# Kernel optimization log

Measured on AMD Instinct MI355X. Metric: run time of the kernel, lower is better.

## Reference

```python
import jax, jax.numpy as jnp
import numpy as np

B, HIMG, WIMG = 8, 24, 24
WIDTH, NCH, CW = 1024, 8, 128
NHEADS, HD = 8, 16
HALF = HD // 2
NFREQ, VOCAB, NCLS = 32, 256, 10
HIDDEN = 4096
EPS = 1e-6
LAMBDA_INIT = 0.8 - 0.6 * float(np.exp(-0.3 * 0.0))  # layer_idx = 0


def rmsnorm(x, w, eps=EPS):
    return x * jax.lax.rsqrt(jnp.mean(x * x, axis=-1, keepdims=True) + eps) * w


def causal_attn(q, k, v, scale):
    # q,k: [B,H,L,d2], v: [B,H,L,D]
    L = q.shape[2]
    scores = jnp.einsum('bhqd,bhkd->bhqk', q, k) * scale
    mask = jnp.tril(jnp.ones((L, L), dtype=bool))
    scores = jnp.where(mask, scores, -jnp.inf)
    return jnp.einsum('bhqk,bhkd->bhqd', jax.nn.softmax(scores, axis=-1), v)


def diff_attn(h, qkv_w, qkv_b, qn_w, kn_w, hn_w, lq1, lk1, lq2, lk2, ow, ob):
    Bb, L, C = h.shape
    qkv = jax.nn.silu(h @ qkv_w + qkv_b).reshape(Bb, L, 3, NHEADS, HD)
    q, k, v = qkv[:, :, 0], qkv[:, :, 1], qkv[:, :, 2]
    t = lambda a: a.transpose(0, 2, 1, 3)  # [B,L,H,d] -> [B,H,L,d]
    q1 = t(rmsnorm(q[..., :HALF], qn_w)); q2 = t(rmsnorm(q[..., HALF:], qn_w))
    k1 = t(rmsnorm(k[..., :HALF], kn_w)); k2 = t(rmsnorm(k[..., HALF:], kn_w))
    v = t(v)
    lam = jnp.exp(jnp.dot(lq1, lk1)) - jnp.exp(jnp.dot(lq2, lk2)) + LAMBDA_INIT
    scale = 1.0 / np.sqrt(HALF)
    out1 = causal_attn(q1, k1, v, scale)
    out2 = causal_attn(q2, k2, v, scale)
    diff = rmsnorm(out1 - lam * out2, hn_w) * (1.0 - LAMBDA_INIT)
    out = diff.transpose(0, 2, 1, 3).reshape(Bb, L, C)
    return jax.nn.silu(out @ ow + ob)


def setup_inputs() -> dict:
    key = jax.random.key(0)
    ks = iter(jax.random.split(key, 64))
    n = lambda shape, s=0.02: jax.random.normal(next(ks), shape, jnp.float32) * s
    return dict(
        x=jax.random.uniform(next(ks), (B, HIMG, WIMG), jnp.float32),
        top_k=4,
        pixel_embed=n((VOCAB, WIDTH)),
        freq_h=n((NFREQ,), 0.1), freq_w=n((NFREQ,), 0.1),
        phase_h=jnp.zeros((NFREQ,), jnp.float32), phase_w=jnp.zeros((NFREQ,), jnp.float32),
        pos_proj_w=n((4 * NFREQ, WIDTH)), pos_proj_b=jnp.zeros((WIDTH,), jnp.float32),
        embed_norm_w=jnp.ones((WIDTH,), jnp.float32),
        se_w1=n((WIDTH, WIDTH // 4)), se_b1=jnp.zeros((WIDTH // 4,), jnp.float32),
        se_w2=n((WIDTH // 4, WIDTH)), se_b2=jnp.zeros((WIDTH,), jnp.float32),
        mix_norm_w=jnp.ones((WIDTH,), jnp.float32),
        mlp_w1=n((WIDTH, HIDDEN)), mlp_b1=jnp.zeros((HIDDEN,), jnp.float32),
        mlp_w2=n((HIDDEN, WIDTH)), mlp_b2=jnp.zeros((WIDTH,), jnp.float32),
        mlp_norm_w=jnp.ones((WIDTH,), jnp.float32),
        router_w=n((WIDTH, NCH)), router_b=jnp.zeros((NCH,), jnp.float32),
        qkv_w=n((NCH, CW, 3 * CW)), qkv_b=jnp.zeros((NCH, 3 * CW), jnp.float32),
        q_norm_w=jnp.ones((NCH, HALF), jnp.float32), k_norm_w=jnp.ones((NCH, HALF), jnp.float32),
        head_norm_w=jnp.ones((NCH, HD), jnp.float32),
        lam_q1=n((NCH, HALF), 0.1), lam_k1=n((NCH, HALF), 0.1),
        lam_q2=n((NCH, HALF), 0.1), lam_k2=n((NCH, HALF), 0.1),
        out_w=n((NCH, CW, CW)), out_b=jnp.zeros((NCH, CW), jnp.float32),
        seg_norm_w=jnp.ones((NCH, CW), jnp.float32),
        head_w=n((WIDTH, NCLS)), head_b=jnp.zeros((NCLS,), jnp.float32),
    )


def reference(x, top_k, pixel_embed, freq_h, freq_w, phase_h, phase_w, pos_proj_w,
              pos_proj_b, embed_norm_w, se_w1, se_b1, se_w2, se_b2, mix_norm_w,
              mlp_w1, mlp_b1, mlp_w2, mlp_b2, mlp_norm_w, router_w, router_b,
              qkv_w, qkv_b, q_norm_w, k_norm_w, head_norm_w, lam_q1, lam_k1,
              lam_q2, lam_k2, out_w, out_b, seg_norm_w, head_w, head_b):
    Bb, H, W = x.shape
    L = H * W
    # LearnedSinusoidal2DEmbed
    hp = jnp.arange(H, dtype=jnp.float32) / H
    wp = jnp.arange(W, dtype=jnp.float32) / W
    fh = jax.nn.softplus(freq_h) * 10.0
    fw = jax.nn.softplus(freq_w) * 10.0
    ha = hp[:, None] * fh + phase_h          # [H, NFREQ]
    wa = wp[:, None] * fw + phase_w
    h_enc = jnp.concatenate([jnp.sin(ha), jnp.cos(ha)], -1)
    w_enc = jnp.concatenate([jnp.sin(wa), jnp.cos(wa)], -1)
    pos = jnp.concatenate([jnp.broadcast_to(h_enc[:, None], (H, W, 2 * NFREQ)),
                           jnp.broadcast_to(w_enc[None, :], (H, W, 2 * NFREQ))], -1)
    pos = pos @ pos_proj_w + pos_proj_b      # [H, W, WIDTH]
    xi = jnp.clip((x * 255.0).astype(jnp.int32), 0, 255).reshape(Bb, L)
    h = pixel_embed[xi] + pos.reshape(1, L, WIDTH)
    h = rmsnorm(h, embed_norm_w)
    # ChannelMixer: SE + RMSNorm residual, MLP residual, top-k router
    s = jnp.mean(h, axis=1)
    s = jax.nn.sigmoid(jax.nn.silu(s @ se_w1 + se_b1) @ se_w2 + se_b2)
    h = h + rmsnorm(h * s[:, None, :] - h, mix_norm_w)
    h = h + rmsnorm(jax.nn.silu(h @ mlp_w1 + mlp_b1) @ mlp_w2 + mlp_b2, mlp_norm_w)
    logits_r = jnp.mean(h, axis=1) @ router_w + router_b   # [B, NCH]
    tv, ti = jax.lax.top_k(logits_r, top_k)
    rw = jnp.zeros_like(logits_r).at[jnp.arange(Bb)[:, None], ti].set(jax.nn.softmax(tv, axis=-1))
    # ChannelSegment: per-channel differential attention expert, routed
    outs = []
    for i in range(NCH):
        hi = h[..., i * CW:(i + 1) * CW]
        o = diff_attn(hi, qkv_w[i], qkv_b[i], q_norm_w[i], k_norm_w[i], head_norm_w[i],
                      lam_q1[i], lam_k1[i], lam_q2[i], lam_k2[i], out_w[i], out_b[i])
        hi = hi + rmsnorm(o, seg_norm_w[i])
        outs.append(hi * rw[:, i][:, None, None])
    h = jnp.concatenate(outs, axis=-1)
    # classifier head
    return jnp.mean(h, axis=1) @ head_w + head_b
```

## Files before the change

kernel.cpp:

```cpp
#include <hip/hip_runtime.h>
#include <math.h>

typedef __bf16 bf16;
typedef __bf16 bf16x8 __attribute__((ext_vector_type(8)));
typedef __bf16 bf16x4 __attribute__((ext_vector_type(4)));
typedef __bf16 bf16x2 __attribute__((ext_vector_type(2)));
typedef float f32x4 __attribute__((ext_vector_type(4)));
typedef short s16x4 __attribute__((ext_vector_type(4)));

constexpr int Bsz = 8, HIMG = 24, WIMG = 24;
constexpr int Lq = 576;
constexpr int WIDTH = 1024, NCH = 8, CW = 128;
constexpr int NHEADS = 8, HD = 16, HALF = 8;
constexpr float EPS = 1e-6f;
constexpr float LAMINIT = 0.2f;
constexpr float QSCALE_E = 0.35355339059327373f * 1.4426950408889634f;
constexpr int ROWS = Bsz * Lq;
constexpr long PSTRIDE = 4718592;

__device__ __forceinline__ float fexp2(float x) {
#if __has_builtin(__builtin_amdgcn_exp2f)
  return __builtin_amdgcn_exp2f(x);
#else
  return exp2f(x);
#endif
}

constexpr size_t B_HB    = 0;
constexpr size_t B_G2B   = B_HB    + 9437184;
constexpr size_t B_ENCB  = B_G2B   + 9437184;
constexpr size_t B_POSWT = B_ENCB  + 163840;
constexpr size_t B_QKVWT = B_POSWT + 262144;
constexpr size_t B_OWT   = B_QKVWT + 786432;
constexpr size_t B_SE    = B_OWT   + 262144;
constexpr size_t B_T1    = B_SE    + 32768;
constexpr size_t B_MP    = B_T1    + 8192;
constexpr size_t B_RW    = B_MP    + 524288;
constexpr size_t B_LAM   = B_RW    + 256;
constexpr size_t B_POOL  = B_LAM   + 256;
constexpr size_t WS_BIG  = B_POOL + 8388608 + 8388608 + 37748736;
constexpr size_t WS_BIG2 = WS_BIG + 9437184;
constexpr size_t WS_BIG3 = WS_BIG + 4 * 9437184;

__device__ __forceinline__ float blockReduceSum256(float v, float* red) {
  #pragma unroll
  for (int off = 32; off; off >>= 1) v += __shfl_down(v, off, 64);
  int lane = threadIdx.x & 63, wid = threadIdx.x >> 6;
  if (lane == 0) red[wid] = v;
  __syncthreads();
  float total = 0.f;
  #pragma unroll
  for (int i = 0; i < 4; i++) total += red[i];
  return total;
}
__device__ __forceinline__ float silu(float x) { return x / (1.f + __expf(-x)); }

__device__ __forceinline__ void gl16(const bf16* g, bf16* l) {
  __builtin_amdgcn_global_load_lds(
      (const __attribute__((address_space(1))) void*)g,
      (__attribute__((address_space(3))) void*)l, 16, 0, 0);
}

__device__ __forceinline__ f32x4 mfma16(bf16x4 a, bf16x4 b, f32x4 c) {
#if __has_builtin(__builtin_amdgcn_mfma_f32_16x16x16bf16_1k)
  union { bf16x4 h; s16x4 s; } ua, ub;
  ua.h = a; ub.h = b;
  return __builtin_amdgcn_mfma_f32_16x16x16bf16_1k(ua.s, ub.s, c, 0, 0, 0);
#else
  f32x4 d = c;
  asm volatile("v_mfma_f32_16x16x16_bf16 %0, %1, %2, %0"
               : "+v"(d) : "v"(a), "v"(b));
  return d;
#endif
}

__device__ __forceinline__ void tcast_tile(const float* __restrict__ W,
    bf16* __restrict__ Wt, int K, int N, long zo, int bx, int by) {
  __shared__ float t[32][33];
  int n0 = bx * 32, k0 = by * 32;
  int tid = threadIdx.x;
  int r = tid >> 3, c4 = (tid & 7) * 4;
  const float4 v = *(const float4*)(W + zo + (long)(k0 + r) * N + n0 + c4);
  t[c4 + 0][r] = v.x; t[c4 + 1][r] = v.y; t[c4 + 2][r] = v.z; t[c4 + 3][r] = v.w;
  __syncthreads();
  bf16* dst = Wt + zo + (long)(n0 + r) * K + k0 + c4;
  dst[0] = (bf16)t[r][c4 + 0]; dst[1] = (bf16)t[r][c4 + 1];
  dst[2] = (bf16)t[r][c4 + 2]; dst[3] = (bf16)t[r][c4 + 3];
}

__global__ __launch_bounds__(256) void k_tcast_all(
    const float* __restrict__ w1, const float* __restrict__ w2,
    const float* __restrict__ posw, const float* __restrict__ qkvw,
    const float* __restrict__ outw,
    bf16* __restrict__ W1T, bf16* __restrict__ W2T, bf16* __restrict__ POSWT,
    bf16* __restrict__ QKVWT, bf16* __restrict__ OWT) {
  int bid = blockIdx.x;
  if (bid < 4096) {
    tcast_tile(w1, W1T, 1024, 4096, 0, bid % 128, bid / 128);
  } else if (bid < 8192) {
    int t = bid - 4096;
    tcast_tile(w2, W2T, 4096, 1024, 0, t % 32, t / 32);
  } else if (bid < 8320) {
    int t = bid - 8192;
    tcast_tile(posw, POSWT, 128, 1024, 0, t % 32, t / 32);
  } else if (bid < 8704) {
    int t = bid - 8320;
    int z = t / 48; t -= z * 48;
    tcast_tile(qkvw, QKVWT, 128, 384, (long)z * 49152, t % 12, t / 12);
  } else {
    int t = bid - 8704;
    int z = t / 16; t -= z * 16;
    tcast_tile(outw, OWT, 128, 128, (long)z * 16384, t % 4, t / 4);
  }
}

__global__ void k_enc_b(const float* __restrict__ fh, const float* __restrict__ fw,
                        const float* __restrict__ ph, const float* __restrict__ pw,
                        bf16* __restrict__ enc) {
  int idx = blockIdx.x * blockDim.x + threadIdx.x;
  if (idx >= Lq * 128) return;
  int l = idx >> 7, c = idx & 127;
  int hh = l / WIMG, ww = l % WIMG;
  float v;
  if (c < 64) {
    int f = c & 31;
    float fr = log1pf(__expf(fh[f])) * 10.f;
    float a = (hh / (float)HIMG) * fr + ph[f];
    v = (c < 32) ? sinf(a) : cosf(a);
  } else {
    int f = c & 31;
    float fr = log1pf(__expf(fw[f])) * 10.f;
    float a = (ww / (float)WIMG) * fr + pw[f];
    v = (c < 96) ? sinf(a) : cosf(a);
  }
  enc[idx] = (bf16)v;
}

template <int ACT, int OUTBF, int SWZ>
__global__ __launch_bounds__(256) void gemm_bt(
    const bf16* __restrict__ A, int lda, long aZs,
    const bf16* __restrict__ Bt, int ldb, long bZs,
    const float* __restrict__ bias, int biasZs,
    void* __restrict__ Cv, int ldc, long cZs,
    int M, int N, int K) {
  __shared__ bf16 As[128 * 32];
  __shared__ bf16 Bs[128 * 32];
  int tid = threadIdx.x;
  int m0, n0, z;
  if constexpr (SWZ == 0) {
    m0 = blockIdx.y * 128; n0 = blockIdx.x * 128; z = blockIdx.z;
  } else if constexpr (SWZ == 1) {
    int lid = blockIdx.x;
    int xcd = lid & 7, idx = lid >> 3;
    int j = idx & 15, G = xcd + 8 * (idx >> 4);
    m0 = (G % 36) * 128; n0 = ((G / 36) * 16 + j) * 128; z = 0;
  } else {
    int lid = blockIdx.x;
    int xcd = lid & 7, idx = lid >> 3;
    int n = idx & 7, G = xcd + 8 * (idx >> 3);
    m0 = (G % 36) * 128; n0 = n * 128; z = G / 36;
  }
  const bf16* Ab = A + (long)z * aZs;
  const bf16* Bb = Bt + (long)z * bZs;
  f32x4 acc[4][4] = {};
  int wv = tid >> 6, lane = tid & 63;
  int wrow = (wv >> 1) * 64, wcol = (wv & 1) * 64;
  int lm = lane & 15, lq = lane >> 4;
  const bf16* ag = Ab + (long)(m0 + (tid >> 2)) * lda + (tid & 3) * 8;
  const bf16* bg = Bb + (long)(n0 + (tid >> 2)) * ldb + (tid & 3) * 8;
  bf16* asd = As + tid * 8;
  bf16* bsd = Bs + tid * 8;
  for (int k0 = 0; k0 < K; k0 += 32) {
    gl16(ag + k0, asd);
    gl16(ag + k0 + 64L * lda, asd + 2048);
    gl16(bg + k0, bsd);
    gl16(bg + k0 + 64L * ldb, bsd + 2048);
    __syncthreads();
    bf16x8 af[4], bfr[4];
    #pragma unroll
    for (int i = 0; i < 4; i++) {
      af[i]  = *(const bf16x8*)(As + (wrow + i * 16 + lm) * 32 + lq * 8);
      bfr[i] = *(const bf16x8*)(Bs + (wcol + i * 16 + lm) * 32 + lq * 8);
    }
    #pragma unroll
    for (int i = 0; i < 4; i++)
      #pragma unroll
      for (int j = 0; j < 4; j++)
        acc[i][j] = __builtin_amdgcn_mfma_f32_16x16x32_bf16(af[i], bfr[j], acc[i][j], 0, 0, 0);
    __syncthreads();
  }
  long cz = (long)z * cZs;
  const float* bz = bias ? bias + (long)z * biasZs : nullptr;
  #pragma unroll
  for (int i = 0; i < 4; i++) {
    int row = m0 + wrow + i * 16 + lq * 4;
    #pragma unroll
    for (int j = 0; j < 4; j++) {
      int col = n0 + wcol + j * 16 + lm;
      float bv = bz ? bz[col] : 0.f;
      #pragma unroll
      for (int r = 0; r < 4; r++) {
        float v = acc[i][j][r] + bv;
        if (ACT == 1) v = silu(v);
        long off = cz + (long)(row + r) * ldc + col;
        if (OUTBF) ((bf16*)Cv)[off] = (bf16)v;
        else       ((float*)Cv)[off] = v;
      }
    }
  }
}

template <int ACT, int OUTBF, int ACC, int NORM>
__global__ __launch_bounds__(256) void gemm64(
    const bf16* __restrict__ A, int lda, long aZs,
    const bf16* __restrict__ Bt, int ldb, long bZs,
    const float* __restrict__ bias, int biasZs,
    void* __restrict__ Cv, int ldc, long cZs,
    int M, int N, int K,
    const float* __restrict__ qn, const float* __restrict__ kn) {
  __shared__ bf16 As[64 * 32];
  __shared__ bf16 Bs[128 * 32];
  int tid = threadIdx.x;
  int m0 = blockIdx.y * 64, n0 = blockIdx.x * 128;
  int z = blockIdx.z;
  const bf16* Ab = A + (long)z * aZs;
  const bf16* Bb = Bt + (long)z * bZs;
  f32x4 acc[4][2] = {};
  int wv = tid >> 6, lane = tid & 63;
  int lm = lane & 15, lq = lane >> 4;
  int wcol = wv * 32;
  const bf16* ag = Ab + (long)(m0 + (tid >> 2)) * lda + (tid & 3) * 8;
  const bf16* bg = Bb + (long)(n0 + (tid >> 2)) * ldb + (tid & 3) * 8;
  bf16* asd = As + tid * 8;
  bf16* bsd = Bs + tid * 8;
  for (int k0 = 0; k0 < K; k0 += 32) {
    gl16(ag + k0, asd);
    gl16(bg + k0, bsd);
    gl16(bg + k0 + 64L * ldb, bsd + 2048);
    __syncthreads();
    bf16x8 af[4], bfr[2];
    #pragma unroll
    for (int i = 0; i < 4; i++)
      af[i] = *(const bf16x8*)(As + (i * 16 + lm) * 32 + lq * 8);
    #pragma unroll
    for (int j = 0; j < 2; j++)
      bfr[j] = *(const bf16x8*)(Bs + (wcol + j * 16 + lm) * 32 + lq * 8);
    #pragma unroll
    for (int i = 0; i < 4; i++)
      #pragma unroll
      for (int j = 0; j < 2; j++)
        acc[i][j] = __builtin_amdgcn_mfma_f32_16x16x32_bf16(af[i], bfr[j], acc[i][j], 0, 0, 0);
    __syncthreads();
  }
  long cz = (long)z * cZs;
  const float* bz = bias ? bias + (long)z * biasZs : nullptr;
  if constexpr (NORM == 0) {
    #pragma unroll
    for (int i = 0; i < 4; i++) {
      int row = m0 + i * 16 + lq * 4;
      #pragma unroll
      for (int j = 0; j < 2; j++) {
        int col = n0 + wcol + j * 16 + lm;
        float bv = bz ? bz[col] : 0.f;
        #pragma unroll
        for (int r = 0; r < 4; r++) {
          float v = acc[i][j][r] + bv;
          long off = cz + (long)(row + r) * ldc + col;
          if (ACC) v += (float)((bf16*)Cv)[off];
          if (ACT == 1) v = silu(v);
          if (OUTBF) ((bf16*)Cv)[off] = (bf16)v;
          else       ((float*)Cv)[off] = v;
        }
      }
    }
  } else {
    int nsec = blockIdx.x;
    bool don = nsec < 2;
    float wnv = 1.f;
    if (nsec == 0) wnv = qn[z * 8 + (lm & 7)] * QSCALE_E;
    else if (nsec == 1) wnv = kn[z * 8 + (lm & 7)];
    #pragma unroll
    for (int i = 0; i < 4; i++) {
      int row = m0 + i * 16 + lq * 4;
      #pragma unroll
      for (int j = 0; j < 2; j++) {
        int col = n0 + wcol + j * 16 + lm;
        float bv = bz ? bz[col] : 0.f;
        #pragma unroll
        for (int r = 0; r < 4; r++) {
          float v = acc[i][j][r] + bv;
          if (ACT == 1) v = silu(v);
          float s = v * v;
          s += __shfl_xor(s, 1);
          s += __shfl_xor(s, 2);
          s += __shfl_xor(s, 4);
          if (don) v = v * rsqrtf(s * 0.125f + EPS) * wnv;
          ((bf16*)Cv)[cz + (long)(row + r) * ldc + col] = (bf16)v;
        }
      }
    }
  }
}

__global__ __launch_bounds__(256) void k_embed(const float* __restrict__ x,
    const float* __restrict__ emb, const float* __restrict__ pos,
    const float* __restrict__ nw, bf16* __restrict__ h) {
  __shared__ float red[4];
  int row = blockIdx.x;
  int l = row % Lq;
  int xi = (int)(x[row] * 255.f);
  xi = min(max(xi, 0), 255);
  const float* er = emb + (long)xi * WIDTH;
  const float* pr = pos + (long)l * WIDTH;
  int c0 = threadIdx.x * 4;
  float v[4]; float ss = 0.f;
  #pragma unroll
  for (int i = 0; i < 4; i++) { v[i] = er[c0 + i] + pr[c0 + i]; ss += v[i] * v[i]; }
  ss = blockReduceSum256(ss, red);
  float r = rsqrtf(ss / WIDTH + EPS);
  bf16* hr = h + (long)row * WIDTH;
  #pragma unroll
  for (int i = 0; i < 4; i++) hr[c0 + i] = (bf16)(v[i] * r * nw[c0 + i]);
}

__global__ void k_meanl_p(const bf16* __restrict__ h, float* __restrict__ part) {
  int lp = blockIdx.x, b = blockIdx.y, t = threadIdx.x;
  const bf16* p = h + ((long)b * Lq + (long)lp * 36) * WIDTH + t * 4;
  float a0 = 0, a1 = 0, a2 = 0, a3 = 0;
  for (int l = 0; l < 36; l++) {
    bf16x4 v = *(const bf16x4*)(p + (long)l * WIDTH);
    a0 += (float)v[0]; a1 += (float)v[1]; a2 += (float)v[2]; a3 += (float)v[3];
  }
  float* dst = part + ((long)b * 16 + lp) * WIDTH + t * 4;
  dst[0] = a0; dst[1] = a1; dst[2] = a2; dst[3] = a3;
}

__global__ __launch_bounds__(256) void k_se1(const float* __restrict__ part,
    const float* __restrict__ w1, const float* __restrict__ b1,
    float* __restrict__ t1) {
  __shared__ float sv[1024];
  __shared__ float red[256];
  int jb = blockIdx.x, b = blockIdx.y, t = threadIdx.x;
  for (int c = t; c < 1024; c += 256) {
    float a = 0.f;
    #pragma unroll
    for (int lp = 0; lp < 16; lp++) a += part[((long)b * 16 + lp) * 1024 + c];
    sv[c] = a * (1.f / 576.f);
  }
  __syncthreads();
  int j = t & 7, pt = t >> 3;
  int j0 = jb * 8;
  float acc = 0.f;
  int c0 = pt * 32;
  #pragma unroll 8
  for (int c = c0; c < c0 + 32; c++) acc += sv[c] * w1[c * 256 + j0 + j];
  red[t] = acc;
  __syncthreads();
  if (t < 8) {
    float a = b1[j0 + t];
    #pragma unroll
    for (int p = 0; p < 32; p++) a += red[p * 8 + t];
    t1[b * 256 + j0 + t] = silu(a);
  }
}

__global__ __launch_bounds__(256) void k_se2(const float* __restrict__ t1,
    const float* __restrict__ w2, const float* __restrict__ b2,
    float* __restrict__ s) {
  __shared__ float red[256];
  int jb = blockIdx.x, b = blockIdx.y, t = threadIdx.x;
  int j = t & 31, pt = t >> 5;
  int j0 = jb * 32;
  const float* tb = t1 + b * 256;
  float acc = 0.f;
  int c0 = pt * 32;
  #pragma unroll 8
  for (int c = c0; c < c0 + 32; c++) acc += tb[c] * w2[c * 1024 + j0 + j];
  red[t] = acc;
  __syncthreads();
  if (t < 32) {
    float a = b2[j0 + t];
    #pragma unroll
    for (int p = 0; p < 8; p++) a += red[p * 32 + t];
    s[b * 1024 + j0 + t] = 1.f / (1.f + __expf(-a));
  }
}

__global__ __launch_bounds__(256) void k_mix_b(bf16* __restrict__ h,
    const float* __restrict__ s, const float* __restrict__ mw) {
  __shared__ float red[4];
  int row = blockIdx.x;
  int b = row / Lq;
  bf16* hr = h + (long)row * WIDTH;
  const float* sb = s + b * WIDTH;
  int c0 = threadIdx.x * 4;
  float hv[4], y[4]; float ss = 0.f;
  #pragma unroll
  for (int i = 0; i < 4; i++) {
    hv[i] = (float)hr[c0 + i];
    y[i] = hv[i] * (sb[c0 + i] - 1.f); ss += y[i] * y[i];
  }
  ss = blockReduceSum256(ss, red);
  float r = rsqrtf(ss / WIDTH + EPS);
  #pragma unroll
  for (int i = 0; i < 4; i++) hr[c0 + i] = (bf16)(hv[i] + y[i] * r * mw[c0 + i]);
}

__global__ __launch_bounds__(256) void k_addnorm_b(bf16* __restrict__ h,
    const bf16* __restrict__ g, const float* __restrict__ mw) {
  __shared__ float red[4];
  int row = blockIdx.x;
  bf16* hr = h + (long)row * WIDTH;
  const bf16* gr = g + (long)row * WIDTH;
  int c0 = threadIdx.x * 4;
  float y[4]; float ss = 0.f;
  #pragma unroll
  for (int i = 0; i < 4; i++) { y[i] = (float)gr[c0 + i]; ss += y[i] * y[i]; }
  ss = blockReduceSum256(ss, red);
  float r = rsqrtf(ss / WIDTH + EPS);
  #pragma unroll
  for (int i = 0; i < 4; i++)
    hr[c0 + i] = (bf16)((float)hr[c0 + i] + y[i] * r * mw[c0 + i]);
}

__global__ __launch_bounds__(256) void k_addnorm2(bf16* __restrict__ h,
    const bf16* __restrict__ p0, const bf16* __restrict__ p1,
    const float* __restrict__ b2, const float* __restrict__ mw) {
  __shared__ float red[4];
  int row = blockIdx.x;
  bf16* hr = h + (long)row * WIDTH;
  const bf16* g0 = p0 + (long)row * WIDTH;
  const bf16* g1 = p1 + (long)row * WIDTH;
  int c0 = threadIdx.x * 4;
  float y[4]; float ss = 0.f;
  #pragma unroll
  for (int i = 0; i < 4; i++) {
    y[i] = (float)g0[c0 + i] + (float)g1[c0 + i] + b2[c0 + i];
    ss += y[i] * y[i];
  }
  ss = blockReduceSum256(ss, red);
  float r = rsqrtf(ss / WIDTH + EPS);
  #pragma unroll
  for (int i = 0; i < 4; i++)
    hr[c0 + i] = (bf16)((float)hr[c0 + i] + y[i] * r * mw[c0 + i]);
}

__global__ __launch_bounds__(256) void k_addnorm4(bf16* __restrict__ h,
    const bf16* __restrict__ parts, const float* __restrict__ b2,
    const float* __restrict__ mw) {
  __shared__ float red[4];
  int row = blockIdx.x;
  bf16* hr = h + (long)row * WIDTH;
  const bf16* g0 = parts + (long)row * WIDTH;
  int c0 = threadIdx.x * 4;
  float y[4]; float ss = 0.f;
  #pragma unroll
  for (int i = 0; i < 4; i++) {
    float a = b2[c0 + i];
    #pragma unroll
    for (int p = 0; p < 4; p++) a += (float)g0[(long)p * PSTRIDE + c0 + i];
    y[i] = a; ss += a * a;
  }
  ss = blockReduceSum256(ss, red);
  float r = rsqrtf(ss / WIDTH + EPS);
  #pragma unroll
  for (int i = 0; i < 4; i++)
    hr[c0 + i] = (bf16)((float)hr[c0 + i] + y[i] * r * mw[c0 + i]);
}

__global__ __launch_bounds__(256) void k_router(const float* __restrict__ part,
    const float* __restrict__ rwgt, const float* __restrict__ rb,
    const float* __restrict__ lq1, const float* __restrict__ lk1,
    const float* __restrict__ lq2, const float* __restrict__ lk2,
    float* __restrict__ rw, float* __restrict__ lam) {
  __shared__ float sv[1024];
  __shared__ float red[256];
  __shared__ float lg[8];
  int b = blockIdx.x, t = threadIdx.x;
  for (int c = t; c < 1024; c += 256) {
    float a = 0.f;
    #pragma unroll
    for (int lp = 0; lp < 16; lp++) a += part[((long)b * 16 + lp) * 1024 + c];
    sv[c] = a * (1.f / 576.f);
  }
  __syncthreads();
  int j = t & 7, pt = t >> 3;
  float acc = 0.f;
  int c0 = pt * 32;
  #pragma unroll 8
  for (int c = c0; c < c0 + 32; c++) acc += sv[c] * rwgt[c * 8 + j];
  red[t] = acc;
  __syncthreads();
  if (t < 8) {
    float a = rb[t];
    for (int p = 0; p < 32; p++) a += red[p * 8 + t];
    lg[t] = a;
  }
  __syncthreads();
  if (t == 0) {
    float v[8]; bool sel[8];
    #pragma unroll
    for (int i = 0; i < 8; i++) { v[i] = lg[i]; sel[i] = false; }
    int idxs[4]; float vals[4];
    for (int s = 0; s < 4; s++) {
      int bi = -1; float bv = -1e30f;
      for (int i = 0; i < 8; i++) if (!sel[i] && v[i] > bv) { bv = v[i]; bi = i; }
      sel[bi] = true; idxs[s] = bi; vals[s] = bv;
    }
    float m = vals[0], den = 0.f, e[4];
    for (int s = 0; s < 4; s++) { e[s] = __expf(vals[s] - m); den += e[s]; }
    for (int i = 0; i < 8; i++) rw[b * 8 + i] = 0.f;
    for (int s = 0; s < 4; s++) rw[b * 8 + idxs[s]] = e[s] / den;
  }
  if (b == 0 && t >= 8 && t < 16) {
    int c = t - 8;
    float d1 = 0.f, d2 = 0.f;
    for (int i = 0; i < 8; i++) {
      d1 += lq1[c * 8 + i] * lk1[c * 8 + i];
      d2 += lq2[c * 8 + i] * lk2[c * 8 + i];
    }
    lam[c] = __expf(d1) - __expf(d2) + LAMINIT;
  }
}

__global__ __launch_bounds__(256) void k_attn_mfma(
    const bf16* __restrict__ qkv, const float* __restrict__ lam,
    const float* __restrict__ hnw, bf16* __restrict__ dc) {
  __shared__ bf16 Ks[576 * 16];
  __shared__ bf16 Vt[16 * 584];
  int tid = threadIdx.x;
  int slice = blockIdx.x; int zc = slice >> 3, b = slice & 7;
  int head = blockIdx.z;
  const bf16* qkvb = qkv + ((long)zc * ROWS + (long)b * Lq) * 384;
  for (int i = tid; i < 1152; i += 256) {
    int row = i >> 1, hf = i & 1;
    gl16(qkvb + (long)row * 384 + 128 + head * 16 + hf * 8, Ks + i * 8);
  }
  for (int i = tid; i < 1152; i += 256) {
    int row = i >> 1, dh = i & 1;
    bf16x8 v = *(const bf16x8*)(qkvb + (long)row * 384 + 256 + head * 16 + dh * 8);
    #pragma unroll
    for (int j = 0; j < 8; j++) Vt[(dh * 8 + j) * 584 + row] = v[j];
  }
  __syncthreads();
  int wv = tid >> 6, lane = tid & 63;
  int lm = lane & 15, lq = lane >> 4;
  float lamv = lam[zc];
  float hwv[4];
  #pragma unroll
  for (int r = 0; r < 4; r++) hwv[r] = hnw[zc * 16 + lq * 4 + r] * (1.f - LAMINIT);
  int u = blockIdx.y * 4 + wv;
  int prA, prB, prC;
  if (u < 6) { prA = u + 2; prB = 17 - u; prC = -1; }
  else       { int v2 = u - 6; prA = v2; prB = 8 + v2; prC = 11 - v2; }
  for (int pi = 0; pi < 3; pi++) {
    int pr = (pi == 0) ? prA : (pi == 1) ? prB : prC;
    if (pr < 0) continue;
    bf16x8 bq0[2] = {{}, {}}, bq1[2] = {{}, {}};
    if (lq < 2) {
      #pragma unroll
      for (int tile = 0; tile < 2; tile++) {
        bf16x8 t8 = *(const bf16x8*)(
            qkvb + (long)(pr * 32 + tile * 16 + lm) * 384 + head * 16 + lq * 8);
        if (lq == 0) bq0[tile] = t8; else bq1[tile] = t8;
      }
    }
    f32x4 o[2][2] = {};
    float den[2][2] = {};
    for (int kc = 0; kc <= pr; kc++) {
      f32x4 sT[2][2][2] = {};
      #pragma unroll
      for (int t = 0; t < 2; t++) {
        bf16x8 aK = {};
        if (lq < 2) aK = *(const bf16x8*)(Ks + (kc * 32 + t * 16 + lm) * 16 + lq * 8);
        #pragma unroll
        for (int tile = 0; tile < 2; tile++) {
          sT[t][tile][0] = __builtin_amdgcn_mfma_f32_16x16x32_bf16(aK, bq0[tile], sT[t][tile][0], 0, 0, 0);
          sT[t][tile][1] = __builtin_amdgcn_mfma_f32_16x16x32_bf16(aK, bq1[tile], sT[t][tile][1], 0, 0, 0);
        }
      }
      bool diag = (kc == pr);
      #pragma unroll
      for (int t = 0; t < 2; t++) {
        bf16x4 aV = *(const bf16x4*)(Vt + lm * 584 + kc * 32 + t * 16 + lq * 4);
        #pragma unroll
        for (int tile = 0; tile < 2; tile++) {
          if (diag && tile == 0 && t == 1) continue;
          bool masked = diag && (tile == t);
          #pragma unroll
          for (int h2 = 0; h2 < 2; h2++) {
            bf16x4 pb;
            float dsum = 0.f;
            #pragma unroll
            for (int r = 0; r < 4; r++) {
              float ev = fexp2(sT[t][tile][h2][r]);
              if (masked && (lq * 4 + r > lm)) ev = 0.f;
              dsum += ev;
              pb[r] = (bf16)ev;
            }
            den[tile][h2] += dsum;
            o[tile][h2] = mfma16(aV, pb, o[tile][h2]);
          }
        }
      }
    }
    #pragma unroll
    for (int tile = 0; tile < 2; tile++)
      #pragma unroll
      for (int h2 = 0; h2 < 2; h2++) {
        den[tile][h2] += __shfl_xor(den[tile][h2], 16);
        den[tile][h2] += __shfl_xor(den[tile][h2], 32);
      }
    #pragma unroll
    for (int tile = 0; tile < 2; tile++) {
      float inv1 = 1.f / den[tile][0];
      float inv2 = lamv / den[tile][1];
      float dff[4]; float ss = 0.f;
      #pragma unroll
      for (int r = 0; r < 4; r++) {
        dff[r] = o[tile][0][r] * inv1 - o[tile][1][r] * inv2;
        ss += dff[r] * dff[r];
      }
      ss += __shfl_xor(ss, 16);
      ss += __shfl_xor(ss, 32);
      float rr = rsqrtf(ss * 0.0625f + EPS);
      bf16x4 outp;
      #pragma unroll
      for (int r = 0; r < 4; r++) outp[r] = (bf16)(dff[r] * rr * hwv[r]);
      long rowg = (long)zc * ROWS + (long)b * Lq + pr * 32 + tile * 16 + lm;
      *(bf16x4*)(dc + rowg * 128 + head * 16 + lq * 4) = outp;
    }
  }
}

__global__ __launch_bounds__(64) void k_segpool(const bf16* __restrict__ h,
    const bf16* __restrict__ op, const float* __restrict__ segw,
    const float* __restrict__ rw, float* __restrict__ part) {
  int lp = blockIdx.x, b = blockIdx.y, ch = blockIdx.z;
  int t = threadIdx.x;
  int c0 = t * 2;
  float w0 = segw[ch * 128 + c0], w1 = segw[ch * 128 + c0 + 1];
  float rwv = rw[b * 8 + ch];
  float a0 = 0.f, a1 = 0.f;
  for (int l = 0; l < 36; l++) {
    int row = b * Lq + lp * 36 + l;
    const bf16* oprow = op + (long)ch * ROWS * CW + (long)row * CW;
    bf16x2 yv = *(const bf16x2*)(oprow + c0);
    float y0 = (float)yv[0], y1 = (float)yv[1];
    float ss = y0 * y0 + y1 * y1;
    #pragma unroll
    for (int m = 1; m < 64; m <<= 1) ss += __shfl_xor(ss, m);
    float r = rsqrtf(ss * (1.f / 128.f) + EPS);
    bf16x2 hv = *(const bf16x2*)(h + (long)row * WIDTH + ch * 128 + c0);
    a0 += ((float)hv[0] + y0 * r * w0) * rwv;
    a1 += ((float)hv[1] + y1 * r * w1) * rwv;
  }
  float* dst = part + ((long)b * 16 + lp) * 1024 + ch * 128 + c0;
  dst[0] = a0; dst[1] = a1;
}

__global__ __launch_bounds__(256) void k_head(const float* __restrict__ part,
    const float* __restrict__ hw, const float* __restrict__ hb, float* __restrict__ out) {
  __shared__ float pool[1024];
  __shared__ float red[256];
  int b = blockIdx.x, t = threadIdx.x;
  for (int c = t; c < 1024; c += 256) {
    float a = 0.f;
    #pragma unroll
    for (int lp = 0; lp < 16; lp++) a += part[((long)b * 16 + lp) * 1024 + c];
    pool[c] = a * (1.f / 576.f);
  }
  __syncthreads();
  int j = t & 15, pt = t >> 4;
  float acc = 0.f;
  if (j < 10)
    for (int c = pt * 64; c < pt * 64 + 64; c++)
      acc += pool[c] * hw[c * 10 + j];
  red[t] = acc;
  __syncthreads();
  if (t < 10) {
    float a = hb[t];
    for (int p = 0; p < 16; p++) a += red[p * 16 + t];
    out[b * 10 + t] = a;
  }
}

extern "C" void kernel_launch(void* const* d_in, const int* in_sizes, int n_in,
                              void* d_out, int out_size, void* d_ws, size_t ws_size,
                              hipStream_t stream) {
  const float* x          = (const float*)d_in[0];
  const float* pixel_embed= (const float*)d_in[2];
  const float* freq_h     = (const float*)d_in[3];
  const float* freq_w     = (const float*)d_in[4];
  const float* phase_h    = (const float*)d_in[5];
  const float* phase_w    = (const float*)d_in[6];
  const float* pos_proj_w = (const float*)d_in[7];
  const float* pos_proj_b = (const float*)d_in[8];
  const float* embed_norm = (const float*)d_in[9];
  const float* se_w1      = (const float*)d_in[10];
  const float* se_b1      = (const float*)d_in[11];
  const float* se_w2      = (const float*)d_in[12];
  const float* se_b2      = (const float*)d_in[13];
  const float* mix_norm   = (const float*)d_in[14];
  const float* mlp_w1     = (const float*)d_in[15];
  const float* mlp_b1     = (const float*)d_in[16];
  const float* mlp_w2     = (const float*)d_in[17];
  const float* mlp_b2     = (const float*)d_in[18];
  const float* mlp_norm   = (const float*)d_in[19];
  const float* router_w   = (const float*)d_in[20];
  const float* router_b   = (const float*)d_in[21];
  const float* qkv_w      = (const float*)d_in[22];
  const float* qkv_b      = (const float*)d_in[23];
  const float* q_norm_w   = (const float*)d_in[24];
  const float* k_norm_w   = (const float*)d_in[25];
  const float* head_norm_w= (const float*)d_in[26];
  const float* lam_q1     = (const float*)d_in[27];
  const float* lam_k1     = (const float*)d_in[28];
  const float* lam_q2     = (const float*)d_in[29];
  const float* lam_k2     = (const float*)d_in[30];
  const float* out_w      = (const float*)d_in[31];
  const float* out_b      = (const float*)d_in[32];
  const float* seg_norm_w = (const float*)d_in[33];
  const float* head_w     = (const float*)d_in[34];
  const float* head_b     = (const float*)d_in[35];

  char* W = (char*)d_ws;
  bf16*  HB    = (bf16*)(W + B_HB);
  bf16*  G2B   = (bf16*)(W + B_G2B);
  float* POS   = (float*)(W + B_G2B);
  bf16*  ENCB  = (bf16*)(W + B_ENCB);
  bf16*  POSWT = (bf16*)(W + B_POSWT);
  bf16*  QKVWT = (bf16*)(W + B_QKVWT);
  bf16*  OWT   = (bf16*)(W + B_OWT);
  float* SE    = (float*)(W + B_SE);
  float* T1    = (float*)(W + B_T1);
  float* MP    = (float*)(W + B_MP);
  float* RW    = (float*)(W + B_RW);
  float* LAM   = (float*)(W + B_LAM);
  char*  P     = W + B_POOL;
  bf16*  W1T   = (bf16*)P;
  bf16*  W2T   = (bf16*)(P + 8388608);
  bf16*  HID   = (bf16*)(P + 16777216);
  bf16*  PARTS = (bf16*)(P + 16777216 + 37748736);
  bf16*  QKV   = (bf16*)P;
  bf16*  DC    = (bf16*)(P + 28311552);
  float* out   = (float*)d_out;
  const int tier = (ws_size >= WS_BIG3) ? 3 : (ws_size >= WS_BIG2) ? 2
                 : (ws_size >= WS_BIG) ? 1 : 0;

  k_tcast_all<<<8832, 256, 0, stream>>>(mlp_w1, mlp_w2, pos_proj_w, qkv_w, out_w,
                                        W1T, W2T, POSWT, QKVWT, OWT);
  k_enc_b<<<288, 256, 0, stream>>>(freq_h, freq_w, phase_h, phase_w, ENCB);
  gemm64<0, 0, 0, 0><<<dim3(8, 10, 1), 256, 0, stream>>>(
      ENCB, 128, 0, POSWT, 128, 0, pos_proj_b, 0, POS, 1024, 0, 640, 1024, 128,
      nullptr, nullptr);
  k_embed<<<ROWS, 256, 0, stream>>>(x, pixel_embed, POS, embed_norm, HB);
  k_meanl_p<<<dim3(16, 8), 256, 0, stream>>>(HB, MP);
  k_se1<<<dim3(32, 8), 256, 0, stream>>>(MP, se_w1, se_b1, T1);
  k_se2<<<dim3(32, 8), 256, 0, stream>>>(T1, se_w2, se_b2, SE);
  k_mix_b<<<ROWS, 256, 0, stream>>>(HB, SE, mix_norm);
  if (tier >= 1) {
    gemm_bt<1, 1, 1><<<1152, 256, 0, stream>>>(
        HB, 1024, 0, W1T, 1024, 0, mlp_b1, 0,
        HID, 4096, 0, 4608, 4096, 1024);
    if (tier == 3) {
      gemm_bt<0, 1, 2><<<1152, 256, 0, stream>>>(
          HID, 4096, 1024, W2T, 4096, 1024, nullptr, 0,
          PARTS, 1024, PSTRIDE, 4608, 1024, 1024);
      k_addnorm4<<<ROWS, 256, 0, stream>>>(HB, PARTS, mlp_b2, mlp_norm);
    } else if (tier == 2) {
      gemm_bt<0, 1, 2><<<576, 256, 0, stream>>>(
          HID, 4096, 2048, W2T, 4096, 2048, nullptr, 0,
          G2B, 1024, (long)(PARTS - G2B), 4608, 1024, 2048);
      k_addnorm2<<<ROWS, 256, 0, stream>>>(HB, G2B, PARTS, mlp_b2, mlp_norm);
    } else {
      gemm64<0, 1, 0, 0><<<dim3(8, 72, 1), 256, 0, stream>>>(
          HID, 4096, 0, W2T, 4096, 0, mlp_b2, 0,
          G2B, 1024, 0, 4608, 1024, 4096, nullptr, nullptr);
      k_addnorm_b<<<ROWS, 256, 0, stream>>>(HB, G2B, mlp_norm);
    }
  } else {
    gemm_bt<1, 1, 0><<<dim3(16, 36, 1), 256, 0, stream>>>(
        HB, 1024, 0, W1T, 1024, 0, mlp_b1, 0, HID, 2048, 0, 4608, 2048, 1024);
    gemm64<0, 1, 0, 0><<<dim3(8, 72, 1), 256, 0, stream>>>(
        HID, 2048, 0, W2T, 4096, 0, mlp_b2, 0, G2B, 1024, 0, 4608, 1024, 2048,
        nullptr, nullptr);
    gemm_bt<1, 1, 0><<<dim3(16, 36, 1), 256, 0, stream>>>(
        HB, 1024, 0, W1T + 2048L * 1024, 1024, 0, mlp_b1 + 2048, 0, HID, 2048, 0,
        4608, 2048, 1024);
    gemm64<0, 1, 1, 0><<<dim3(8, 72, 1), 256, 0, stream>>>(
        HID, 2048, 0, W2T + 2048, 4096, 0, nullptr, 0, G2B, 1024, 0,
        4608, 1024, 2048, nullptr, nullptr);
    k_addnorm_b<<<ROWS, 256, 0, stream>>>(HB, G2B, mlp_norm);
  }
  k_meanl_p<<<dim3(16, 8), 256, 0, stream>>>(HB, MP);
  k_router<<<8, 256, 0, stream>>>(MP, router_w, router_b,
                                  lam_q1, lam_k1, lam_q2, lam_k2, RW, LAM);
  gemm64<1, 1, 0, 1><<<dim3(3, 72, 8), 256, 0, stream>>>(
      HB, 1024, CW, QKVWT, 128, 384 * 128, qkv_b, 384,
      QKV, 384, (long)ROWS * 384, ROWS, 384, 128, q_norm_w, k_norm_w);
  k_attn_mfma<<<dim3(64, 2, 8), 256, 0, stream>>>(QKV, LAM, head_norm_w, DC);
  gemm64<1, 1, 0, 0><<<dim3(1, 72, 8), 256, 0, stream>>>(
      DC, 128, (long)ROWS * 128, OWT, 128, 128 * 128, out_b, 128,
      DC, 128, (long)ROWS * 128, ROWS, 128, 128, nullptr, nullptr);
  k_segpool<<<dim3(16, 8, 8), 64, 0, stream>>>(HB, DC, seg_norm_w, RW, MP);
  k_head<<<8, 256, 0, stream>>>(MP, head_w, head_b, out);
}
```

Baseline: 443.7 us.

## Add 256x256-tile double-buffered MFMA GEMM for MLP layers with remainder tail

```diff
diff --git a/kernel.cpp b/kernel.cpp
--- a/kernel.cpp
+++ b/kernel.cpp
@@ -205,6 +205,152 @@
         long off = cz + (long)(row + r) * ldc + col;
         if (OUTBF) ((bf16*)Cv)[off] = (bf16)v;
         else       ((float*)Cv)[off] = v;
+      }
+    }
+  }
+}
+
+template <int ACT>
+__global__ __launch_bounds__(512) void gemm256(
+    const bf16* __restrict__ A, int lda, long aZs,
+    const bf16* __restrict__ Bt, int ldb, long bZs,
+    const float* __restrict__ bias,
+    bf16* __restrict__ C, int ldc, long cZs,
+    int Mtiles, int Ntiles, int K) {
+  __shared__ bf16 LDS[65536];
+  const int tid = threadIdx.x;
+  const int cpx = gridDim.x >> 3;
+  const int wg = (blockIdx.x & 7) * cpx + (blockIdx.x >> 3);
+  const int per_z = Mtiles * Ntiles;
+  const int z = wg / per_z, rwg = wg % per_z;
+  const int m0 = (rwg / Ntiles) * 256, n0 = (rwg % Ntiles) * 256;
+  const bf16* Ab = A + (long)z * aZs;
+  const bf16* Bb = Bt + (long)z * bZs;
+  const int c0 = tid, c1 = tid + 512;
+  const int sr0 = c0 >> 3, sc0 = ((c0 & 7) ^ (sr0 & 7)) * 8;
+  const int sr1 = c1 >> 3, sc1 = ((c1 & 7) ^ (sr1 & 7)) * 8;
+  const long a00 = (long)(m0 + sr0) * lda + sc0;
+  const long a01 = (long)(m0 + sr1) * lda + sc1;
+  const long a10 = (long)(m0 + 128 + sr0) * lda + sc0;
+  const long a11 = (long)(m0 + 128 + sr1) * lda + sc1;
+  const long b00 = (long)(n0 + sr0) * ldb + sc0;
+  const long b01 = (long)(n0 + sr1) * ldb + sc1;
+  const long b10 = (long)(n0 + 128 + sr0) * ldb + sc0;
+  const long b11 = (long)(n0 + 128 + sr1) * ldb + sc1;
+  const int d0 = c0 * 8, d1 = c1 * 8;
+  auto stage = [&](int kt, int buf) {
+    const bf16* Ak = Ab + kt * 64;
+    const bf16* Bk = Bb + kt * 64;
+    bf16* L = LDS + buf * 32768;
+    gl16(Ak + a00, L + d0);         gl16(Ak + a01, L + d1);
+    gl16(Ak + a10, L + 8192 + d0);  gl16(Ak + a11, L + 8192 + d1);
+    gl16(Bk + b00, L + 16384 + d0); gl16(Bk + b01, L + 16384 + d1);
+    gl16(Bk + b10, L + 24576 + d0); gl16(Bk + b11, L + 24576 + d1);
+  };
+  const int wv = tid >> 6, lane = tid & 63;
+  const int wm = wv >> 2, wn = wv & 3;
+  const int lm = lane & 15, lq = lane >> 4;
+  const int sw = lm & 7;
+  const int abase = wm * 8192;
+  const int bbase = 16384 + (wn >> 1) * 8192;
+  const int brow0 = (wn & 1) * 64;
+  const int kq0 = (lq ^ sw) * 8;
+  const int kq1 = ((4 + lq) ^ sw) * 8;
+  f32x4 acc[8][4] = {};
+  bf16x8 afr[4][2], bfr[2][2];
+  const int NT = K >> 6;
+  stage(0, 0);
+  asm volatile("s_waitcnt vmcnt(0)" ::: "memory");
+  __builtin_amdgcn_s_barrier();
+  for (int s = 0; s < NT; ++s) {
+    const int bb = (s & 1) * 32768;
+    const bf16* La = LDS + bb + abase + lm * 64;
+    const bf16* Lb = LDS + bb + bbase + (brow0 + lm) * 64;
+    #pragma unroll
+    for (int f = 0; f < 4; f++) {
+      afr[f][0] = *(const bf16x8*)(La + f * 1024 + kq0);
+      afr[f][1] = *(const bf16x8*)(La + f * 1024 + kq1);
+    }
+    #pragma unroll
+    for (int g = 0; g < 2; g++) {
+      bfr[g][0] = *(const bf16x8*)(Lb + g * 1024 + kq0);
+      bfr[g][1] = *(const bf16x8*)(Lb + g * 1024 + kq1);
+    }
+    if (s + 1 < NT) stage(s + 1, ((s & 1) ^ 1));
+    __builtin_amdgcn_s_barrier();
+    __builtin_amdgcn_s_setprio(1);
+    #pragma unroll
+    for (int f = 0; f < 4; f++)
+      #pragma unroll
+      for (int g = 0; g < 2; g++) {
+        acc[f][g] = __builtin_amdgcn_mfma_f32_16x16x32_bf16(afr[f][0], bfr[g][0], acc[f][g], 0, 0, 0);
+        acc[f][g] = __builtin_amdgcn_mfma_f32_16x16x32_bf16(afr[f][1], bfr[g][1], acc[f][g], 0, 0, 0);
+      }
+    __builtin_amdgcn_s_setprio(0);
+    __builtin_amdgcn_s_barrier();
+    #pragma unroll
+    for (int g = 0; g < 2; g++) {
+      bfr[g][0] = *(const bf16x8*)(Lb + 2048 + g * 1024 + kq0);
+      bfr[g][1] = *(const bf16x8*)(Lb + 2048 + g * 1024 + kq1);
+    }
+    __builtin_amdgcn_s_barrier();
+    __builtin_amdgcn_s_setprio(1);
+    #pragma unroll
+    for (int f = 0; f < 4; f++)
+      #pragma unroll
+      for (int g = 0; g < 2; g++) {
+        acc[f][2 + g] = __builtin_amdgcn_mfma_f32_16x16x32_bf16(afr[f][0], bfr[g][0], acc[f][2 + g], 0, 0, 0);
+        acc[f][2 + g] = __builtin_amdgcn_mfma_f32_16x16x32_bf16(afr[f][1], bfr[g][1], acc[f][2 + g], 0, 0, 0);
+      }
+    __builtin_amdgcn_s_setprio(0);
+    __builtin_amdgcn_s_barrier();
+    #pragma unroll
+    for (int f = 0; f < 4; f++) {
+      afr[f][0] = *(const bf16x8*)(La + 4096 + f * 1024 + kq0);
+      afr[f][1] = *(const bf16x8*)(La + 4096 + f * 1024 + kq1);
+    }
+    __builtin_amdgcn_s_barrier();
+    __builtin_amdgcn_s_setprio(1);
+    #pragma unroll
+    for (int f = 0; f < 4; f++)
+      #pragma unroll
+      for (int g = 0; g < 2; g++) {
+        acc[4 + f][2 + g] = __builtin_amdgcn_mfma_f32_16x16x32_bf16(afr[f][0], bfr[g][0], acc[4 + f][2 + g], 0, 0, 0);
+        acc[4 + f][2 + g] = __builtin_amdgcn_mfma_f32_16x16x32_bf16(afr[f][1], bfr[g][1], acc[4 + f][2 + g], 0, 0, 0);
+      }
+    __builtin_amdgcn_s_setprio(0);
+    __builtin_amdgcn_s_barrier();
+    #pragma unroll
+    for (int g = 0; g < 2; g++) {
+      bfr[g][0] = *(const bf16x8*)(Lb + g * 1024 + kq0);
+      bfr[g][1] = *(const bf16x8*)(Lb + g * 1024 + kq1);
+    }
+    __builtin_amdgcn_s_barrier();
+    __builtin_amdgcn_s_setprio(1);
+    #pragma unroll
+    for (int f = 0; f < 4; f++)
+      #pragma unroll
+      for (int g = 0; g < 2; g++) {
+        acc[4 + f][g] = __builtin_amdgcn_mfma_f32_16x16x32_bf16(afr[f][0], bfr[g][0], acc[4 + f][g], 0, 0, 0);
+        acc[4 + f][g] = __builtin_amdgcn_mfma_f32_16x16x32_bf16(afr[f][1], bfr[g][1], acc[4 + f][g], 0, 0, 0);
+      }
+    __builtin_amdgcn_s_setprio(0);
+    if (s + 1 < NT) { asm volatile("s_waitcnt vmcnt(0)" ::: "memory"); }
+    __builtin_amdgcn_s_barrier();
+  }
+  const long cz = (long)z * cZs;
+  #pragma unroll
+  for (int i = 0; i < 8; i++) {
+    const int row = m0 + wm * 128 + (i >> 2) * 64 + (i & 3) * 16 + lq * 4;
+    #pragma unroll
+    for (int j = 0; j < 4; j++) {
+      const int col = n0 + wn * 64 + (j >> 1) * 32 + (j & 1) * 16 + lm;
+      const float bv = bias ? bias[col] : 0.f;
+      #pragma unroll
+      for (int rr = 0; rr < 4; rr++) {
+        float v = acc[i][j][rr] + bv;
+        if (ACT == 1) v = silu(v);
+        C[cz + (long)(row + rr) * ldc + col] = (bf16)v;
       }
     }
   }
@@ -760,13 +906,19 @@
   k_se2<<<dim3(32, 8), 256, 0, stream>>>(T1, se_w2, se_b2, SE);
   k_mix_b<<<ROWS, 256, 0, stream>>>(HB, SE, mix_norm);
   if (tier >= 1) {
-    gemm_bt<1, 1, 1><<<1152, 256, 0, stream>>>(
-        HB, 1024, 0, W1T, 1024, 0, mlp_b1, 0,
-        HID, 4096, 0, 4608, 4096, 1024);
+    gemm256<1><<<256, 512, 0, stream>>>(
+        HB, 1024, 0, W1T, 1024, 0, mlp_b1,
+        HID, 4096, 0, 16, 16, 1024);
+    gemm_bt<1, 1, 0><<<dim3(32, 4, 1), 256, 0, stream>>>(
+        HB + 4096L * 1024, 1024, 0, W1T, 1024, 0, mlp_b1, 0,
+        HID + 4096L * 4096, 4096, 0, 512, 4096, 1024);
     if (tier == 3) {
-      gemm_bt<0, 1, 2><<<1152, 256, 0, stream>>>(
-          HID, 4096, 1024, W2T, 4096, 1024, nullptr, 0,
-          PARTS, 1024, PSTRIDE, 4608, 1024, 1024);
+      gemm256<0><<<256, 512, 0, stream>>>(
+          HID, 4096, 1024, W2T, 4096, 1024, nullptr,
+          PARTS, 1024, PSTRIDE, 16, 4, 1024);
+      gemm_bt<0, 1, 0><<<dim3(8, 4, 4), 256, 0, stream>>>(
+          HID + 4096L * 4096, 4096, 1024, W2T, 4096, 1024, nullptr, 0,
+          PARTS + 4096L * 1024, 1024, PSTRIDE, 512, 1024, 1024);
       k_addnorm4<<<ROWS, 256, 0, stream>>>(HB, PARTS, mlp_b2, mlp_norm);
     } else if (tier == 2) {
       gemm_bt<0, 1, 2><<<576, 256, 0, stream>>>(
```

Result: no change. 451.6 us (+1.8%).
